# Optimization experiments

Measured on AMD Instinct MI355X. Metric: run time of the kernel, lower is better.

## Reference

```python
import jax, jax.numpy as jnp
import numpy as np

D = 128
EMB = 1024
B, S = 4, 4096


def setup_inputs() -> dict:
    key = jax.random.key(0)
    ks = jax.random.split(key, 7)
    scale = 1.0 / np.sqrt(EMB)
    return {
        "X": jax.random.normal(ks[0], (B, S, EMB), dtype=jnp.float32),
        "lam": jnp.float32(0.8),
        "Wq": jax.random.uniform(ks[1], (EMB, 2 * D), jnp.float32, -scale, scale),
        "bq": jax.random.uniform(ks[2], (2 * D,), jnp.float32, -scale, scale),
        "Wk": jax.random.uniform(ks[3], (EMB, 2 * D), jnp.float32, -scale, scale),
        "bk": jax.random.uniform(ks[4], (2 * D,), jnp.float32, -scale, scale),
        "Wv": jax.random.uniform(ks[5], (EMB, D), jnp.float32, -scale, scale),
        "bv": jax.random.uniform(ks[6], (D,), jnp.float32, -scale, scale),
    }


def reference(X, lam, Wq, bq, Wk, bk, Wv, bv):
    # Projections: Q,K are [B,S,2d]; V is [B,S,d]
    Q = X @ Wq + bq
    K = X @ Wk + bk
    V = X @ Wv + bv
    Q1, Q2 = Q[..., :D], Q[..., D:]
    K1, K2 = K[..., :D], K[..., D:]
    s = 1.0 / jnp.sqrt(jnp.float32(D))
    # Dual QK^T scores [B,S,S]
    A1 = jnp.einsum("bqd,bkd->bqk", Q1, K1) * s
    A2 = jnp.einsum("bqd,bkd->bqk", Q2, K2) * s
    P = jax.nn.softmax(A1, axis=-1) - lam * jax.nn.softmax(A2, axis=-1)
    return jnp.einsum("bqk,bkd->bqd", P, V)
```

## Files before the change

### kernel.cpp

```cpp
#include <hip/hip_runtime.h>
#include <hip/hip_bf16.h>


typedef __attribute__((ext_vector_type(8))) short bf16x8;
typedef __attribute__((ext_vector_type(4))) float f32x4;
typedef __attribute__((ext_vector_type(16))) float f32x16;

#define MFMA16(a, b, c) __builtin_amdgcn_mfma_f32_16x16x32_bf16((a), (b), (c), 0, 0, 0)
#define MFMA32(a, b, c) __builtin_amdgcn_mfma_f32_32x32x16_bf16((a), (b), (c), 0, 0, 0)

__device__ __forceinline__ unsigned short f2bf(float x) {
    union { float f; unsigned u; } v; v.f = x;
    return (unsigned short)((v.u + 0x7FFFu + ((v.u >> 16) & 1u)) >> 16);
}
__device__ __forceinline__ unsigned pk2bf(float a, float b) {
    __hip_bfloat162 h = __float22bfloat162_rn(float2{a, b});
    union { __hip_bfloat162 h2; unsigned u; } cv; cv.h2 = h;
    return cv.u;
}

__global__ __launch_bounds__(256) void wtrans_kernel(
    const float* __restrict__ Wq, const float* __restrict__ Wk,
    const float* __restrict__ Wv, unsigned short* __restrict__ Wt) {
    int tid = blockIdx.x * 256 + threadIdx.x;
    int k = tid & 1023, n = tid >> 10;
    float v;
    if (n < 256)      v = Wq[k * 256 + n];
    else if (n < 512) v = Wk[k * 256 + (n - 256)];
    else              v = Wv[k * 128 + (n - 512)];
    Wt[tid] = f2bf(v);
}

__global__ __launch_bounds__(256) void proj_kernel(
    const float* __restrict__ X, const unsigned short* __restrict__ Wt,
    const float* __restrict__ bq, const float* __restrict__ bk,
    const float* __restrict__ bv,
    unsigned short* __restrict__ Qs, unsigned short* __restrict__ Kb,
    unsigned short* __restrict__ Vb) {
    __shared__ alignas(16) char lds[16384];
    const int nt = blockIdx.y;
    const int m0 = blockIdx.x * 128;
    const int t = threadIdx.x, w = t >> 6, l = t & 63, c = l & 15, g = l >> 4;
    const int wm = w >> 1, wn = w & 1;
    const unsigned short* Wrow = Wt + (long)(nt * 128) * 1024;

    f32x4 acc[4][4];
    const f32x4 fz = {0.f, 0.f, 0.f, 0.f};
#pragma unroll
    for (int i = 0; i < 4; i++)
#pragma unroll
        for (int j = 0; j < 4; j++) acc[i][j] = fz;

    const int srow = t >> 1, sh = t & 1;
    const int sswz = (srow & 7) << 4;
    for (int k0 = 0; k0 < 1024; k0 += 32) {
        const float* xs = X + (long)(m0 + srow) * 1024 + k0 + sh * 16;
        float4 f0 = *(const float4*)(xs + 0);
        float4 f1 = *(const float4*)(xs + 4);
        float4 f2 = *(const float4*)(xs + 8);
        float4 f3 = *(const float4*)(xs + 12);
        const unsigned short* wsc = Wrow + (long)srow * 1024 + k0 + sh * 16;
        uint4 w0 = *(const uint4*)(wsc + 0);
        uint4 w1 = *(const uint4*)(wsc + 8);
        uint4 xa, xb;
        xa.x = pk2bf(f0.x, f0.y); xa.y = pk2bf(f0.z, f0.w);
        xa.z = pk2bf(f1.x, f1.y); xa.w = pk2bf(f1.z, f1.w);
        xb.x = pk2bf(f2.x, f2.y); xb.y = pk2bf(f2.z, f2.w);
        xb.z = pk2bf(f3.x, f3.y); xb.w = pk2bf(f3.z, f3.w);
        int base = srow * 64 + sh * 32;
        *(uint4*)(lds + ((base + 0) ^ sswz)) = xa;
        *(uint4*)(lds + ((base + 16) ^ sswz)) = xb;
        *(uint4*)(lds + 8192 + ((base + 0) ^ sswz)) = w0;
        *(uint4*)(lds + 8192 + ((base + 16) ^ sswz)) = w1;
        __syncthreads();

        bf16x8 af[4];
#pragma unroll
        for (int am = 0; am < 4; am++) {
            int r_ = wm * 64 + am * 16 + c;
            af[am] = *(const bf16x8*)(lds + ((r_ * 64 + g * 16) ^ ((c & 7) << 4)));
        }
#pragma unroll
        for (int bn = 0; bn < 4; bn++) {
            int r_ = wn * 64 + bn * 16 + c;
            bf16x8 bfr = *(const bf16x8*)(lds + 8192 + ((r_ * 64 + g * 16) ^ ((c & 7) << 4)));
#pragma unroll
            for (int am = 0; am < 4; am++) acc[am][bn] = MFMA16(af[am], bfr, acc[am][bn]);
        }
        __syncthreads();
    }

    const float QSCALE = 0.08838834764831845f * 1.4426950408889634f;
    const float* bias; float scale; unsigned short* outp; int ostride, ocol0, boff;
    if (nt < 2)      { bias = bq; boff = nt * 128;       scale = QSCALE; outp = Qs; ostride = 256; ocol0 = nt * 128; }
    else if (nt < 4) { bias = bk; boff = (nt - 2) * 128; scale = 1.0f;   outp = Kb; ostride = 256; ocol0 = (nt - 2) * 128; }
    else             { bias = bv; boff = 0;              scale = 1.0f;   outp = Vb; ostride = 128; ocol0 = 0; }
#pragma unroll
    for (int bn = 0; bn < 4; bn++) {
        int ncol = wn * 64 + bn * 16 + c;
        float bb = bias[boff + ncol];
#pragma unroll
        for (int am = 0; am < 4; am++) {
#pragma unroll
            for (int r = 0; r < 4; r++) {
                long row = m0 + wm * 64 + am * 16 + 4 * g + r;
                outp[row * ostride + ocol0 + ncol] = f2bf((acc[am][bn][r] + bb) * scale);
            }
        }
    }
}

__global__ __launch_bounds__(256) void vtrans_kernel(
    const unsigned short* __restrict__ Vb, unsigned short* __restrict__ Vt) {
    int tid = blockIdx.x * 256 + threadIdx.x;
    int s = tid & 4095, d = (tid >> 12) & 127, b = tid >> 19;
    Vt[tid] = Vb[(((long)b << 12) + s) * 128 + d];
}

__global__ __launch_bounds__(512) void attn2_kernel(
    const unsigned short* __restrict__ Qs, const unsigned short* __restrict__ Kb,
    const unsigned short* __restrict__ Vt,
    float* __restrict__ Po, float* __restrict__ Ps, int nsplit, int ks) {
    __shared__ alignas(16) char lds[24576];
    const int t = threadIdx.x;
    const int w = t >> 6, l = t & 63, r31 = l & 31, hi = l >> 5;
    const int wq = w >> 1, br = w & 1;

    const int total = gridDim.x;
    const int lin = (blockIdx.x & 7) * (total >> 3) + (blockIdx.x >> 3);
    const int grp = lin >> 5, qb = lin & 31;
    const int b = grp / nsplit, split = grp % nsplit;

    const long qrow = (long)b * 4096 + qb * 128 + wq * 32 + r31;
    bf16x8 qf[8];
    const unsigned short* Qp = Qs + qrow * 256 + br * 128 + hi * 8;
#pragma unroll
    for (int ds = 0; ds < 8; ds++) qf[ds] = *(const bf16x8*)(Qp + ds * 16);

    f32x16 o[4];
    const f32x16 oz = {};
#pragma unroll
    for (int dt = 0; dt < 4; dt++) o[dt] = oz;
    float m = -1e30f, s = 0.f;

    const int krow = t >> 4, kseg = t & 15, khalf = kseg >> 3;
    char* kdst = lds + khalf * 8192;
    const int koff = krow * 256 + (kseg & 7) * 32;
    const int kxor = ((krow & 7) << 4) ^ (khalf << 5);
    const int vrow = t >> 2, vq = t & 3;
    const unsigned short* vsrc = Vt + (((long)b * 128 + vrow) << 12);
    const int voff = (vrow * 64 + vq * 16) ^ ((vrow & 7) << 4);
    const long kbb = (long)b * 4096;

    const int kb0 = split * ks, kend = kb0 + ks;
    uint4 kr0, kr1, vr0;
    {
        const unsigned short* kp = Kb + (kbb + kb0 + krow) * 256 + kseg * 16;
        kr0 = *(const uint4*)(kp);
        kr1 = *(const uint4*)(kp + 8);
        vr0 = *(const uint4*)(vsrc + kb0 + vq * 8);
    }

    const int krd_sw = ((r31 & 7) << 4) ^ (br << 5);
    const char* kbase = lds + br * 8192;

    for (int kb = kb0; kb < kend; kb += 32) {
        __syncthreads();
        *(uint4*)(kdst + ((koff + 0) ^ kxor)) = kr0;
        *(uint4*)(kdst + ((koff + 16) ^ kxor)) = kr1;
        *(uint4*)(lds + 16384 + voff) = vr0;
        __syncthreads();
        {
            int kn = (kb + 32 < kend) ? kb + 32 : kb0;
            const unsigned short* kp = Kb + (kbb + kn + krow) * 256 + kseg * 16;
            kr0 = *(const uint4*)(kp);
            kr1 = *(const uint4*)(kp + 8);
            vr0 = *(const uint4*)(vsrc + kn + vq * 8);
        }

        f32x16 p = oz;
#pragma unroll
        for (int ds = 0; ds < 8; ds++) {
            bf16x8 kf = *(const bf16x8*)(kbase + ((r31 * 256 + ds * 32 + hi * 16) ^ krd_sw));
            p = MFMA32(kf, qf[ds], p);
        }

        float lmx = p[0];
#pragma unroll
        for (int i = 1; i < 16; i++) lmx = fmaxf(lmx, p[i]);
        lmx = fmaxf(lmx, __shfl_xor(lmx, 32));
        if (__any(lmx > m + 8.f)) {
            float mn = fmaxf(m, lmx);
            float al = exp2f(m - mn);
            s *= al; m = mn;
#pragma unroll
            for (int dt = 0; dt < 4; dt++) o[dt] *= al;
        }
        float pe[16];
#pragma unroll
        for (int i = 0; i < 16; i++) pe[i] = exp2f(p[i] - m);
        float ps_ = 0.f;
#pragma unroll
        for (int i = 0; i < 16; i++) ps_ += pe[i];
        ps_ += __shfl_xor(ps_, 32);
        s += ps_;

        unsigned cA = pk2bf(pe[0], pe[1]), cB = pk2bf(pe[2], pe[3]);
        unsigned cC = pk2bf(pe[4], pe[5]), cD = pk2bf(pe[6], pe[7]);
        asm volatile("v_permlane32_swap_b32 %0, %1" : "+v"(cA), "+v"(cC));
        asm volatile("v_permlane32_swap_b32 %0, %1" : "+v"(cB), "+v"(cD));
        unsigned dA = pk2bf(pe[8], pe[9]), dB = pk2bf(pe[10], pe[11]);
        unsigned dC = pk2bf(pe[12], pe[13]), dD = pk2bf(pe[14], pe[15]);
        asm volatile("v_permlane32_swap_b32 %0, %1" : "+v"(dA), "+v"(dC));
        asm volatile("v_permlane32_swap_b32 %0, %1" : "+v"(dB), "+v"(dD));
        union { uint4 u; bf16x8 v; } pb0, pb1;
        pb0.u = uint4{cA, cB, cC, cD};
        pb1.u = uint4{dA, dB, dC, dD};

#pragma unroll
        for (int dt = 0; dt < 4; dt++) {
            int vr = dt * 32 + r31;
            int vsw = (vr & 7) << 4;
            bf16x8 vf0 = *(const bf16x8*)(lds + 16384 + ((vr * 64 + hi * 16) ^ vsw));
            bf16x8 vf1 = *(const bf16x8*)(lds + 16384 + ((vr * 64 + 32 + hi * 16) ^ vsw));
            o[dt] = MFMA32(vf0, pb0.v, o[dt]);
            o[dt] = MFMA32(vf1, pb1.v, o[dt]);
        }
    }

    float* po = Po + (((qrow)*nsplit + split) * 2 + br) * 128;
#pragma unroll
    for (int dt = 0; dt < 4; dt++) {
#pragma unroll
        for (int rg = 0; rg < 4; rg++) {
            float4 v;
            v.x = o[dt][rg * 4 + 0];
            v.y = o[dt][rg * 4 + 1];
            v.z = o[dt][rg * 4 + 2];
            v.w = o[dt][rg * 4 + 3];
            *(float4*)(po + dt * 32 + rg * 8 + hi * 4) = v;
        }
    }
    if (hi == 0)
        *(float2*)(Ps + (qrow * nsplit + split) * 4 + br * 2) = float2{m, s};
}

__global__ __launch_bounds__(256) void combine_kernel(
    const float* __restrict__ Po, const float* __restrict__ Ps,
    const float* __restrict__ lam_p, float* __restrict__ out, int nsplit) {
    int tid = blockIdx.x * 256 + threadIdx.x;
    int q = tid >> 5, dq = (tid & 31) * 4;
    float M1 = -1e30f, M2 = -1e30f;
    for (int s = 0; s < nsplit; s++) {
        float4 st = *(const float4*)(Ps + (long)(q * nsplit + s) * 4);
        M1 = fmaxf(M1, st.x); M2 = fmaxf(M2, st.z);
    }
    float S1 = 0.f, S2 = 0.f;
    float a0 = 0.f, a1 = 0.f, a2 = 0.f, a3 = 0.f;
    float b0 = 0.f, b1 = 0.f, b2 = 0.f, b3 = 0.f;
    for (int s = 0; s < nsplit; s++) {
        float4 st = *(const float4*)(Ps + (long)(q * nsplit + s) * 4);
        float w1 = exp2f(st.x - M1), w2 = exp2f(st.z - M2);
        S1 += st.y * w1; S2 += st.w * w2;
        const float* p1 = Po + (((long)q * nsplit + s) * 2 + 0) * 128 + dq;
        const float* p2 = Po + (((long)q * nsplit + s) * 2 + 1) * 128 + dq;
        float4 v1 = *(const float4*)p1;
        float4 v2 = *(const float4*)p2;
        a0 += v1.x * w1; a1 += v1.y * w1; a2 += v1.z * w1; a3 += v1.w * w1;
        b0 += v2.x * w2; b1 += v2.y * w2; b2 += v2.z * w2; b3 += v2.w * w2;
    }
    float lam = *lam_p;
    float i1 = 1.f / S1, i2 = lam / S2;
    float4 v;
    v.x = a0 * i1 - b0 * i2;
    v.y = a1 * i1 - b1 * i2;
    v.z = a2 * i1 - b2 * i2;
    v.w = a3 * i1 - b3 * i2;
    *(float4*)(out + (long)q * 128 + dq) = v;
}

extern "C" void kernel_launch(void* const* d_in, const int* in_sizes, int n_in,
                              void* d_out, int out_size, void* d_ws, size_t ws_size,
                              hipStream_t stream) {
    const float* X   = (const float*)d_in[0];
    const float* lam = (const float*)d_in[1];
    const float* Wq  = (const float*)d_in[2];
    const float* bq  = (const float*)d_in[3];
    const float* Wk  = (const float*)d_in[4];
    const float* bk  = (const float*)d_in[5];
    const float* Wv  = (const float*)d_in[6];
    const float* bv  = (const float*)d_in[7];
    char* ws = (char*)d_ws;
    unsigned short* Qs = (unsigned short*)(ws);
    unsigned short* Kb = (unsigned short*)(ws + (8u << 20));
    unsigned short* Vb = (unsigned short*)(ws + (16u << 20));
    unsigned short* Vt = (unsigned short*)(ws + (20u << 20));
    unsigned short* Wt = (unsigned short*)(ws + (24u << 20));
    const size_t base = (size_t)26 << 20;
    const size_t NQ = 16384;
    int nsplit = 1;
    if (ws_size >= base + NQ * 4 * 2 * 128 * 4 + NQ * 4 * 4 * 4)      nsplit = 4;
    else if (ws_size >= base + NQ * 2 * 2 * 128 * 4 + NQ * 2 * 4 * 4) nsplit = 2;
    float* Po = (float*)(ws + base);
    float* Ps = (float*)(ws + base + NQ * (size_t)nsplit * 2 * 128 * 4);

    wtrans_kernel<<<2560, 256, 0, stream>>>(Wq, Wk, Wv, Wt);
    proj_kernel<<<dim3(128, 5), 256, 0, stream>>>(X, Wt, bq, bk, bv, Qs, Kb, Vb);
    vtrans_kernel<<<8192, 256, 0, stream>>>(Vb, Vt);
    attn2_kernel<<<128 * nsplit, 512, 0, stream>>>(Qs, Kb, Vt, Po, Ps,
                                                   nsplit, 4096 / nsplit);
    combine_kernel<<<2048, 256, 0, stream>>>(Po, Ps, lam, (float*)d_out, nsplit);
}
```

Measured before the change: 187.7 us.

## Double-buffer K/V tiles in LDS and use raw v_exp_f32 in attention

The attention kernel now keeps two LDS buffers for the K/V tiles, doubling shared memory to 48KB. Each iteration writes the next tile into the other buffer while computing on the current one, so one of the two __syncthreads per iteration goes away. It also replaces exp2f with a raw v_exp_f32 instruction, splits the QK MFMA chain into two independent accumulators, and uses tree reductions for max and sum. The extra LDS can lower occupancy, and the raw exp skips the range handling that exp2f performs for denormals.

```diff
diff --git a/kernel.cpp b/kernel.cpp
--- a/kernel.cpp
+++ b/kernel.cpp
@@ -17,6 +17,9 @@
     __hip_bfloat162 h = __float22bfloat162_rn(float2{a, b});
     union { __hip_bfloat162 h2; unsigned u; } cv; cv.h2 = h;
     return cv.u;
+}
+__device__ __forceinline__ float fexp2(float x) {
+    float r; asm("v_exp_f32 %0, %1" : "=v"(r) : "v"(x)); return r;
 }
 
 __global__ __launch_bounds__(256) void wtrans_kernel(
@@ -121,7 +124,7 @@
     const unsigned short* __restrict__ Qs, const unsigned short* __restrict__ Kb,
     const unsigned short* __restrict__ Vt,
     float* __restrict__ Po, float* __restrict__ Ps, int nsplit, int ks) {
-    __shared__ alignas(16) char lds[24576];
+    __shared__ alignas(16) char lds[49152];
     const int t = threadIdx.x;
     const int w = t >> 6, l = t & 63, r31 = l & 31, hi = l >> 5;
     const int wq = w >> 1, br = w & 1;
@@ -144,64 +147,84 @@
     float m = -1e30f, s = 0.f;
 
     const int krow = t >> 4, kseg = t & 15, khalf = kseg >> 3;
-    char* kdst = lds + khalf * 8192;
-    const int koff = krow * 256 + (kseg & 7) * 32;
-    const int kxor = ((krow & 7) << 4) ^ (khalf << 5);
+    const int kdoff = khalf * 8192 + (((krow * 256 + (kseg & 7) * 32)) ^
+                                      (((krow & 7) << 4) ^ (khalf << 5)));
     const int vrow = t >> 2, vq = t & 3;
     const unsigned short* vsrc = Vt + (((long)b * 128 + vrow) << 12);
-    const int voff = (vrow * 64 + vq * 16) ^ ((vrow & 7) << 4);
+    const int voff = 16384 + ((vrow * 64 + vq * 16) ^ ((vrow & 7) << 4));
     const long kbb = (long)b * 4096;
 
     const int kb0 = split * ks, kend = kb0 + ks;
     uint4 kr0, kr1, vr0;
+#define LOADTILE(KN)                                                        \
+    {                                                                       \
+        const unsigned short* kp = Kb + (kbb + (KN) + krow) * 256 + kseg * 16; \
+        kr0 = *(const uint4*)(kp);                                          \
+        kr1 = *(const uint4*)(kp + 8);                                      \
+        vr0 = *(const uint4*)(vsrc + (KN) + vq * 8);                        \
+    }
+#define WRITETILE(BUF)                                                      \
+    {                                                                       \
+        char* bb_ = lds + (BUF)*24576;                                      \
+        *(uint4*)(bb_ + kdoff) = kr0;                                       \
+        *(uint4*)(bb_ + (kdoff ^ 16)) = kr1;                                \
+        *(uint4*)(bb_ + voff) = vr0;                                        \
+    }
+
+    LOADTILE(kb0);
+    WRITETILE(0);
     {
-        const unsigned short* kp = Kb + (kbb + kb0 + krow) * 256 + kseg * 16;
-        kr0 = *(const uint4*)(kp);
-        kr1 = *(const uint4*)(kp + 8);
-        vr0 = *(const uint4*)(vsrc + kb0 + vq * 8);
+        int kn = (kb0 + 32 < kend) ? kb0 + 32 : kb0;
+        LOADTILE(kn);
     }
 
     const int krd_sw = ((r31 & 7) << 4) ^ (br << 5);
-    const char* kbase = lds + br * 8192;
+    const int kbofs = br * 8192;
+    int cur = 0;
 
     for (int kb = kb0; kb < kend; kb += 32) {
         __syncthreads();
-        *(uint4*)(kdst + ((koff + 0) ^ kxor)) = kr0;
-        *(uint4*)(kdst + ((koff + 16) ^ kxor)) = kr1;
-        *(uint4*)(lds + 16384 + voff) = vr0;
-        __syncthreads();
-        {
-            int kn = (kb + 32 < kend) ? kb + 32 : kb0;
-            const unsigned short* kp = Kb + (kbb + kn + krow) * 256 + kseg * 16;
-            kr0 = *(const uint4*)(kp);
-            kr1 = *(const uint4*)(kp + 8);
-            vr0 = *(const uint4*)(vsrc + kn + vq * 8);
-        }
-
-        f32x16 p = oz;
-#pragma unroll
-        for (int ds = 0; ds < 8; ds++) {
-            bf16x8 kf = *(const bf16x8*)(kbase + ((r31 * 256 + ds * 32 + hi * 16) ^ krd_sw));
-            p = MFMA32(kf, qf[ds], p);
-        }
-
-        float lmx = p[0];
-#pragma unroll
-        for (int i = 1; i < 16; i++) lmx = fmaxf(lmx, p[i]);
+        if (kb + 32 < kend) {
+            WRITETILE(cur ^ 1);
+            int kn = (kb + 64 < kend) ? kb + 64 : kb0;
+            LOADTILE(kn);
+        }
+        const char* bufp = lds + cur * 24576;
+        const char* kbase = bufp + kbofs;
+
+        f32x16 pa = oz, pb_ = oz;
+#pragma unroll
+        for (int ds = 0; ds < 4; ds++) {
+            bf16x8 kfa = *(const bf16x8*)(kbase + ((r31 * 256 + ds * 32 + hi * 16) ^ krd_sw));
+            bf16x8 kfb = *(const bf16x8*)(kbase + ((r31 * 256 + (ds + 4) * 32 + hi * 16) ^ krd_sw));
+            pa = MFMA32(kfa, qf[ds], pa);
+            pb_ = MFMA32(kfb, qf[ds + 4], pb_);
+        }
+        f32x16 p;
+#pragma unroll
+        for (int i = 0; i < 16; i++) p[i] = pa[i] + pb_[i];
+
+        float x0 = fmaxf(fmaxf(p[0], p[1]), fmaxf(p[2], p[3]));
+        float x1 = fmaxf(fmaxf(p[4], p[5]), fmaxf(p[6], p[7]));
+        float x2 = fmaxf(fmaxf(p[8], p[9]), fmaxf(p[10], p[11]));
+        float x3 = fmaxf(fmaxf(p[12], p[13]), fmaxf(p[14], p[15]));
+        float lmx = fmaxf(fmaxf(x0, x1), fmaxf(x2, x3));
         lmx = fmaxf(lmx, __shfl_xor(lmx, 32));
         if (__any(lmx > m + 8.f)) {
             float mn = fmaxf(m, lmx);
-            float al = exp2f(m - mn);
+            float al = fexp2(m - mn);
             s *= al; m = mn;
 #pragma unroll
             for (int dt = 0; dt < 4; dt++) o[dt] *= al;
         }
         float pe[16];
 #pragma unroll
-        for (int i = 0; i < 16; i++) pe[i] = exp2f(p[i] - m);
-        float ps_ = 0.f;
-#pragma unroll
-        for (int i = 0; i < 16; i++) ps_ += pe[i];
+        for (int i = 0; i < 16; i++) pe[i] = fexp2(p[i] - m);
+        float s0 = (pe[0] + pe[1]) + (pe[2] + pe[3]);
+        float s1 = (pe[4] + pe[5]) + (pe[6] + pe[7]);
+        float s2 = (pe[8] + pe[9]) + (pe[10] + pe[11]);
+        float s3 = (pe[12] + pe[13]) + (pe[14] + pe[15]);
+        float ps_ = (s0 + s1) + (s2 + s3);
         ps_ += __shfl_xor(ps_, 32);
         s += ps_;
 
@@ -221,11 +244,12 @@
         for (int dt = 0; dt < 4; dt++) {
             int vr = dt * 32 + r31;
             int vsw = (vr & 7) << 4;
-            bf16x8 vf0 = *(const bf16x8*)(lds + 16384 + ((vr * 64 + hi * 16) ^ vsw));
-            bf16x8 vf1 = *(const bf16x8*)(lds + 16384 + ((vr * 64 + 32 + hi * 16) ^ vsw));
+            bf16x8 vf0 = *(const bf16x8*)(bufp + 16384 + ((vr * 64 + hi * 16) ^ vsw));
+            bf16x8 vf1 = *(const bf16x8*)(bufp + 16384 + ((vr * 64 + 32 + hi * 16) ^ vsw));
             o[dt] = MFMA32(vf0, pb0.v, o[dt]);
             o[dt] = MFMA32(vf1, pb1.v, o[dt]);
         }
+        cur ^= 1;
     }
 
     float* po = Po + (((qrow)*nsplit + split) * 2 + br) * 128;
@@ -260,7 +284,7 @@
     float b0 = 0.f, b1 = 0.f, b2 = 0.f, b3 = 0.f;
     for (int s = 0; s < nsplit; s++) {
         float4 st = *(const float4*)(Ps + (long)(q * nsplit + s) * 4);
-        float w1 = exp2f(st.x - M1), w2 = exp2f(st.z - M2);
+        float w1 = fexp2(st.x - M1), w2 = fexp2(st.z - M2);
         S1 += st.y * w1; S2 += st.w * w2;
         const float* p1 = Po + (((long)q * nsplit + s) * 2 + 0) * 128 + dq;
         const float* p2 = Po + (((long)q * nsplit + s) * 2 + 1) * 128 + dq;
```

After: 172.6 us. -8.1%, faster.
